# Optimization experiments

Measured on AMD Instinct MI355X. Metric: run time of the kernel, lower is better.

## Reference

```python
import math
import jax, jax.numpy as jnp
import numpy as np

N_HEAD = 16

def setup_inputs() -> dict:
    key = jax.random.key(0)
    k1, k2, k3 = jax.random.split(key, 3)
    B, T, C = 4, 2048, 1024
    x = jax.random.normal(k1, (B, T, C), dtype=jnp.float32)
    Wqkv = jax.random.normal(k2, (C, 3 * C), dtype=jnp.float32) * (1.0 / math.sqrt(C))
    bqkv = jnp.zeros((3 * C,), dtype=jnp.float32)
    Wproj = jax.random.normal(k3, (C, C), dtype=jnp.float32) * (1.0 / math.sqrt(C))
    bproj = jnp.zeros((C,), dtype=jnp.float32)
    return {"x": x, "Wqkv": Wqkv, "bqkv": bqkv, "Wproj": Wproj, "bproj": bproj}

def reference(x, Wqkv, bqkv, Wproj, bproj):
    B, T, C = x.shape
    H = N_HEAD
    D = C // H
    # fused QKV projection
    qkv = x @ Wqkv + bqkv                      # [B,T,3C]
    qkv = qkv.reshape(B, T, 3, H, D).transpose(0, 2, 3, 1, 4)  # [B,3,H,T,D]
    q, k, v = qkv[:, 0], qkv[:, 1], qkv[:, 2]  # each [B,H,T,D]
    scale = 1.0 / math.sqrt(D)
    att = jnp.einsum('bhtd,bhsd->bhts', q, k) * scale  # [B,H,T,T]
    # causal mask: disallow s > t
    mask = jnp.triu(jnp.ones((T, T), dtype=bool), k=1)
    att = jnp.where(mask, jnp.float32(-1e9), att)
    att = jax.nn.softmax(att, axis=-1)
    y = jnp.einsum('bhts,bhsd->bhtd', att, v)  # [B,H,T,D]
    y = y.transpose(0, 2, 1, 3).reshape(B, T, C)
    y = y @ Wproj + bproj
    return y
```

## Files before the change

kernel.cpp:

```cpp
#include <hip/hip_runtime.h>
#include <hip/hip_bf16.h>

#define B_ 4
#define T_ 2048
#define C_ 1024
#define H_ 16
#define D_ 64

typedef __attribute__((ext_vector_type(8))) short short8;
typedef __attribute__((ext_vector_type(4))) float f32x4;

#define QSCALE 0.18033688011112042f

static __device__ __forceinline__ unsigned short f2bf(float f) {
  unsigned u = __float_as_uint(f);
  u += 0x7fff + ((u >> 16) & 1);
  return (unsigned short)(u >> 16);
}

static __device__ __forceinline__ unsigned cvt_pk_bf16(float lo, float hi) {
  unsigned r;
  asm("v_cvt_pk_bf16_f32 %0, %1, %2" : "=v"(r) : "v"(lo), "v"(hi));
  return r;
}

static __device__ __forceinline__ float fast_exp2(float x) {
#if __has_builtin(__builtin_amdgcn_exp2f)
  return __builtin_amdgcn_exp2f(x);
#else
  return exp2f(x);
#endif
}

#define GL2LDS16(g, l)                                              \
  __builtin_amdgcn_global_load_lds(                                 \
      (const __attribute__((address_space(1))) void*)(g),           \
      (__attribute__((address_space(3))) void*)(l), 16, 0, 0)

__global__ __launch_bounds__(256) void prepass(
    const float* __restrict__ x, const float* __restrict__ Wq,
    const float* __restrict__ Wp, ushort* __restrict__ xb,
    ushort* __restrict__ Wqt, ushort* __restrict__ Wpt) {
  __shared__ ushort tile[32][33];
  const int bid = blockIdx.x;
  if (bid < 8192) {
    const size_t i = ((size_t)bid * 256 + threadIdx.x) * 4;
    float4 vv = *(const float4*)(x + i);
    ushort4 o = {f2bf(vv.x), f2bf(vv.y), f2bf(vv.z), f2bf(vv.w)};
    *(ushort4*)(xb + i) = o;
    return;
  }
  const float* in;
  ushort* out;
  int N, tix;
  if (bid < 8192 + 3072) {
    in = Wq; out = Wqt; N = 3 * C_; tix = bid - 8192;
  } else {
    in = Wp; out = Wpt; N = C_; tix = bid - 11264;
  }
  const int nT = N >> 5;
  const int k0 = (tix / nT) << 5, n0 = (tix % nT) << 5;
  const int r = threadIdx.x >> 3;
  const int c4 = (threadIdx.x & 7) << 2;
  float4 v = *(const float4*)(in + (size_t)(k0 + r) * N + n0 + c4);
  tile[c4 + 0][r] = f2bf(v.x);
  tile[c4 + 1][r] = f2bf(v.y);
  tile[c4 + 2][r] = f2bf(v.z);
  tile[c4 + 3][r] = f2bf(v.w);
  __syncthreads();
  ushort4 o = {tile[r][c4], tile[r][c4 + 1], tile[r][c4 + 2], tile[r][c4 + 3]};
  *(ushort4*)(out + (size_t)(n0 + r) * C_ + k0 + c4) = o;
}

static __device__ __forceinline__ void swz_src64(int wave, int lane, int p,
                                                 int& row, int& offU) {
  const int flat = p * 4096 + wave * 1024 + lane * 16;
  row = flat >> 7;
  const int pos = (flat & 127) >> 4;
  const int x = pos ^ (row & 7);
  offU = x * 8;
}
static __device__ __forceinline__ int swz_frag64(int r, int quad, int ko) {
  return r * 128 + (((quad | (ko << 2)) ^ (r & 7)) << 4);
}

__global__ __launch_bounds__(256) void gemm_qkv_mfma(
    const ushort* __restrict__ A, const ushort* __restrict__ Bt,
    const float* __restrict__ bias, ushort* __restrict__ q,
    ushort* __restrict__ k, ushort* __restrict__ v) {
  __shared__ __align__(16) ushort As[128 * 64];
  __shared__ __align__(16) ushort Bs[128 * 64];
  const int tid = threadIdx.x;
  const int wave = tid >> 6, lane = tid & 63;
  const int c = lane & 15, quad = lane >> 4;
  const int wm = wave & 1, wn = wave >> 1;
  const int bid0 = blockIdx.y * 24 + blockIdx.x;
  const int bid = (bid0 & 7) * 192 + (bid0 >> 3);
  const int m0 = (bid / 24) << 7;
  const int n0 = (bid % 24) << 7;

  int sRow[4], sOff[4];
#pragma unroll
  for (int p = 0; p < 4; ++p) swz_src64(wave, lane, p, sRow[p], sOff[p]);
  int fOffA[2][4], fOffB[2][4];
#pragma unroll
  for (int ko = 0; ko < 2; ++ko) {
#pragma unroll
    for (int i = 0; i < 4; ++i)
      fOffA[ko][i] = swz_frag64(wm * 64 + i * 16 + c, quad, ko);
#pragma unroll
    for (int j = 0; j < 4; ++j)
      fOffB[ko][j] = swz_frag64(wn * 64 + j * 16 + c, quad, ko);
  }

  f32x4 acc[4][4];
#pragma unroll
  for (int i = 0; i < 4; ++i)
#pragma unroll
    for (int j = 0; j < 4; ++j) acc[i][j] = (f32x4){0.f, 0.f, 0.f, 0.f};

  for (int k0 = 0; k0 < C_; k0 += 64) {
    __syncthreads();
#pragma unroll
    for (int p = 0; p < 4; ++p) {
      GL2LDS16(A + (size_t)(m0 + sRow[p]) * C_ + k0 + sOff[p],
               (char*)As + p * 4096 + wave * 1024);
      GL2LDS16(Bt + (size_t)(n0 + sRow[p]) * C_ + k0 + sOff[p],
               (char*)Bs + p * 4096 + wave * 1024);
    }
    __syncthreads();
#pragma unroll
    for (int ko = 0; ko < 2; ++ko) {
      short8 af[4], bf[4];
#pragma unroll
      for (int i = 0; i < 4; ++i)
        af[i] = *(const short8*)((const char*)As + fOffA[ko][i]);
#pragma unroll
      for (int j = 0; j < 4; ++j)
        bf[j] = *(const short8*)((const char*)Bs + fOffB[ko][j]);
#pragma unroll
      for (int i = 0; i < 4; ++i)
#pragma unroll
        for (int j = 0; j < 4; ++j)
          acc[i][j] = __builtin_amdgcn_mfma_f32_16x16x32_bf16(af[i], bf[j],
                                                              acc[i][j], 0, 0, 0);
    }
  }

  const int s = n0 >> 10;
  if (s == 2) {
#pragma unroll
    for (int j = 0; j < 4; ++j) {
      const int n = n0 + wn * 64 + j * 16 + c;
      const int h = (n >> 6) & 15, d = n & 63;
      const float bval = bias[n];
#pragma unroll
      for (int i = 0; i < 4; ++i) {
        const int m = m0 + wm * 64 + i * 16 + quad * 4;
        const int b = m >> 11, t = m & 2047;
        ushort4 pk = {f2bf(acc[i][j][0] + bval), f2bf(acc[i][j][1] + bval),
                      f2bf(acc[i][j][2] + bval), f2bf(acc[i][j][3] + bval)};
        *(ushort4*)(v + (((size_t)((b << 4) + h) << 6) + d) * T_ + t) = pk;
      }
    }
  } else {
    ushort* outp = (s == 0) ? q : k;
    const float sc = (s == 0) ? QSCALE : 1.0f;
#pragma unroll
    for (int j = 0; j < 4; ++j) {
      const int n = n0 + wn * 64 + j * 16 + c;
      const int h = (n >> 6) & 15, d = n & 63;
      const float bval = bias[n];
#pragma unroll
      for (int i = 0; i < 4; ++i) {
#pragma unroll
        for (int r = 0; r < 4; ++r) {
          const int m = m0 + wm * 64 + i * 16 + quad * 4 + r;
          const int b = m >> 11, t = m & 2047;
          outp[(((size_t)((b << 4) + h) << 11) + t) * 64 + d] =
              f2bf((acc[i][j][r] + bval) * sc);
        }
      }
    }
  }
}

__global__ __launch_bounds__(256) void gemm_proj_mfma(
    const ushort* __restrict__ A, const ushort* __restrict__ Bt,
    const float* __restrict__ bias, float* __restrict__ out) {
  __shared__ __align__(16) ushort As[128 * 64];
  __shared__ __align__(16) ushort Bs[128 * 64];
  const int tid = threadIdx.x;
  const int wave = tid >> 6, lane = tid & 63;
  const int c = lane & 15, quad = lane >> 4;
  const int wm = wave & 1, wn = wave >> 1;
  const int bid0 = blockIdx.y * 8 + blockIdx.x;
  const int bid = (bid0 & 7) * 64 + (bid0 >> 3);
  const int m0 = (bid >> 3) << 7;
  const int n0 = (bid & 7) << 7;

  int sRow[4], sOff[4];
#pragma unroll
  for (int p = 0; p < 4; ++p) swz_src64(wave, lane, p, sRow[p], sOff[p]);
  int fOffA[2][4], fOffB[2][4];
#pragma unroll
  for (int ko = 0; ko < 2; ++ko) {
#pragma unroll
    for (int i = 0; i < 4; ++i)
      fOffA[ko][i] = swz_frag64(wm * 64 + i * 16 + c, quad, ko);
#pragma unroll
    for (int j = 0; j < 4; ++j)
      fOffB[ko][j] = swz_frag64(wn * 64 + j * 16 + c, quad, ko);
  }

  f32x4 acc[4][4];
#pragma unroll
  for (int i = 0; i < 4; ++i)
#pragma unroll
    for (int j = 0; j < 4; ++j) acc[i][j] = (f32x4){0.f, 0.f, 0.f, 0.f};

  for (int k0 = 0; k0 < C_; k0 += 64) {
    __syncthreads();
#pragma unroll
    for (int p = 0; p < 4; ++p) {
      GL2LDS16(A + (size_t)(m0 + sRow[p]) * C_ + k0 + sOff[p],
               (char*)As + p * 4096 + wave * 1024);
      GL2LDS16(Bt + (size_t)(n0 + sRow[p]) * C_ + k0 + sOff[p],
               (char*)Bs + p * 4096 + wave * 1024);
    }
    __syncthreads();
#pragma unroll
    for (int ko = 0; ko < 2; ++ko) {
      short8 af[4], bf[4];
#pragma unroll
      for (int i = 0; i < 4; ++i)
        af[i] = *(const short8*)((const char*)As + fOffA[ko][i]);
#pragma unroll
      for (int j = 0; j < 4; ++j)
        bf[j] = *(const short8*)((const char*)Bs + fOffB[ko][j]);
#pragma unroll
      for (int i = 0; i < 4; ++i)
#pragma unroll
        for (int j = 0; j < 4; ++j)
          acc[i][j] = __builtin_amdgcn_mfma_f32_16x16x32_bf16(af[i], bf[j],
                                                              acc[i][j], 0, 0, 0);
    }
  }

#pragma unroll
  for (int j = 0; j < 4; ++j) {
    const int n = n0 + wn * 64 + j * 16 + c;
    const float bval = bias[n];
#pragma unroll
    for (int i = 0; i < 4; ++i) {
#pragma unroll
      for (int r = 0; r < 4; ++r) {
        const int m = m0 + wm * 64 + i * 16 + quad * 4 + r;
        out[(size_t)m * C_ + n] = acc[i][j][r] + bval;
      }
    }
  }
}

__global__ __launch_bounds__(256) void attn(const ushort* __restrict__ q,
                                            const ushort* __restrict__ k,
                                            const ushort* __restrict__ v,
                                            ushort* __restrict__ y2) {
  const int qt = 15 - (int)(blockIdx.x >> 6);
  const int bh = blockIdx.x & 63;
  const int t0 = qt << 7;
  const int w = threadIdx.x >> 6;
  const int lane = threadIdx.x & 63;
  const int c = lane & 15;
  const int quad = lane >> 4;

  const ushort* qp = q + (size_t)bh * T_ * D_;
  const ushort* kp = k + (size_t)bh * T_ * D_;
  const ushort* vp = v + (size_t)bh * D_ * T_;

  __shared__ __align__(16) ushort Ks[2][64 * 64];
  __shared__ __align__(16) ushort Vs[2][64 * 64];
  __shared__ __align__(16) ushort Ps[4][32][72];

  short8 qf[2][2];
#pragma unroll
  for (int g = 0; g < 2; ++g) {
    const ushort* qrow = qp + (size_t)(t0 + 32 * w + 16 * g + c) * D_;
    qf[g][0] = *(const short8*)(qrow + quad * 8);
    qf[g][1] = *(const short8*)(qrow + 32 + quad * 8);
  }

  int sRow[2], sX[2];
#pragma unroll
  for (int p = 0; p < 2; ++p) {
    const int flat = p * 4096 + (int)threadIdx.x * 16;
    sRow[p] = flat >> 7;
    sX[p] = (((flat & 127) >> 4) ^ (sRow[p] & 7)) * 8;
  }

#define STAGE(buf, s0s)                                                   \
  do {                                                                    \
    _Pragma("unroll") for (int p = 0; p < 2; ++p) {                       \
      GL2LDS16(kp + (size_t)((s0s) + sRow[p]) * D_ + sX[p],               \
               (char*)Ks[buf] + p * 4096 + w * 1024);                     \
      GL2LDS16(vp + (size_t)sRow[p] * T_ + (s0s) + sX[p],                 \
               (char*)Vs[buf] + p * 4096 + w * 1024);                     \
    }                                                                     \
  } while (0)

  f32x4 o[2][4];
  float l_i[2] = {0.f, 0.f};
#pragma unroll
  for (int g = 0; g < 2; ++g)
#pragma unroll
    for (int dt = 0; dt < 4; ++dt) o[g][dt] = (f32x4){0.f, 0.f, 0.f, 0.f};

  const int nb = 2 * qt + 2;
  STAGE(0, 0);
  int cur = 0;

  for (int ib = 0; ib < nb; ++ib) {
    const int s0 = ib << 6;
    __syncthreads();
    if (ib + 1 < nb) STAGE(cur ^ 1, s0 + 64);

    f32x4 st[2][4];
    __builtin_amdgcn_s_setprio(1);
#pragma unroll
    for (int kt = 0; kt < 4; ++kt) {
      const char* kb = (const char*)Ks[cur];
      short8 af0 = *(const short8*)(kb + swz_frag64(kt * 16 + c, quad, 0));
      short8 af1 = *(const short8*)(kb + swz_frag64(kt * 16 + c, quad, 1));
#pragma unroll
      for (int g = 0; g < 2; ++g) {
        f32x4 a = (f32x4){0.f, 0.f, 0.f, 0.f};
        a = __builtin_amdgcn_mfma_f32_16x16x32_bf16(af0, qf[g][0], a, 0, 0, 0);
        a = __builtin_amdgcn_mfma_f32_16x16x32_bf16(af1, qf[g][1], a, 0, 0, 0);
        st[g][kt] = a;
      }
    }
    __builtin_amdgcn_s_setprio(0);

#pragma unroll
    for (int g = 0; g < 2; ++g) {
      const int qbase = t0 + 32 * w + 16 * g;
      if (s0 + 63 > qbase) {
#pragma unroll
        for (int kt = 0; kt < 4; ++kt)
#pragma unroll
          for (int r = 0; r < 4; ++r)
            if (s0 + kt * 16 + 4 * quad + r > qbase + c) st[g][kt][r] = -1e30f;
      }
      float lacc = 0.f;
#pragma unroll
      for (int kt = 0; kt < 4; ++kt) {
        float p0 = fast_exp2(st[g][kt][0]);
        float p1 = fast_exp2(st[g][kt][1]);
        float p2 = fast_exp2(st[g][kt][2]);
        float p3 = fast_exp2(st[g][kt][3]);
        lacc += (p0 + p1) + (p2 + p3);
        uint2 pw = {cvt_pk_bf16(p0, p1), cvt_pk_bf16(p2, p3)};
        *(uint2*)(&Ps[w][g * 16 + c][kt * 16 + 4 * quad]) = pw;
      }
      l_i[g] += lacc;
    }

    short8 pf[2][2];
#pragma unroll
    for (int g = 0; g < 2; ++g) {
      pf[g][0] = *(const short8*)(&Ps[w][g * 16 + c][quad * 8]);
      pf[g][1] = *(const short8*)(&Ps[w][g * 16 + c][32 + quad * 8]);
    }
    __builtin_amdgcn_s_setprio(1);
#pragma unroll
    for (int dt = 0; dt < 4; ++dt) {
      const char* vb = (const char*)Vs[cur];
      short8 vf0 = *(const short8*)(vb + swz_frag64(dt * 16 + c, quad, 0));
      short8 vf1 = *(const short8*)(vb + swz_frag64(dt * 16 + c, quad, 1));
#pragma unroll
      for (int g = 0; g < 2; ++g) {
        o[g][dt] =
            __builtin_amdgcn_mfma_f32_16x16x32_bf16(vf0, pf[g][0], o[g][dt], 0, 0, 0);
        o[g][dt] =
            __builtin_amdgcn_mfma_f32_16x16x32_bf16(vf1, pf[g][1], o[g][dt], 0, 0, 0);
      }
    }
    __builtin_amdgcn_s_setprio(0);
    cur ^= 1;
  }
#undef STAGE

  float linv[2];
#pragma unroll
  for (int g = 0; g < 2; ++g) {
    float ls = l_i[g];
    ls += __shfl_xor(ls, 16);
    ls += __shfl_xor(ls, 32);
    linv[g] = 1.0f / ls;
  }

  const int b = bh >> 4, h = bh & 15;
#pragma unroll
  for (int g = 0; g < 2; ++g) {
    const int row = t0 + 32 * w + 16 * g + c;
    ushort* dst = y2 + (size_t)(b * T_ + row) * C_ + h * 64;
#pragma unroll
    for (int dt = 0; dt < 4; ++dt) {
      uint2 ov = {cvt_pk_bf16(o[g][dt][0] * linv[g], o[g][dt][1] * linv[g]),
                  cvt_pk_bf16(o[g][dt][2] * linv[g], o[g][dt][3] * linv[g])};
      *(uint2*)(dst + dt * 16 + 4 * quad) = ov;
    }
  }
}

extern "C" void kernel_launch(void* const* d_in, const int* in_sizes, int n_in,
                              void* d_out, int out_size, void* d_ws,
                              size_t ws_size, hipStream_t stream) {
  const float* x = (const float*)d_in[0];
  const float* Wqkv = (const float*)d_in[1];
  const float* bqkv = (const float*)d_in[2];
  const float* Wproj = (const float*)d_in[3];
  const float* bproj = (const float*)d_in[4];
  float* out = (float*)d_out;

  const size_t per = (size_t)B_ * H_ * T_ * D_;
  ushort* q = (ushort*)d_ws;
  ushort* k = q + per;
  ushort* v = k + per;
  ushort* y2 = v + per;
  ushort* xb = y2 + per;
  ushort* Wqkvt = xb + per;
  ushort* Wprojt = Wqkvt + 3 * C_ * C_;

  prepass<<<dim3(12288), 256, 0, stream>>>(x, Wqkv, Wproj, xb, Wqkvt, Wprojt);
  gemm_qkv_mfma<<<dim3(24, 64), 256, 0, stream>>>(xb, Wqkvt, bqkv, q, k, v);
  attn<<<dim3(1024), 256, 0, stream>>>(q, k, v, y2);
  gemm_proj_mfma<<<dim3(8, 64), 256, 0, stream>>>(y2, Wprojt, bproj, out);
}
```

Before: 244.2 us.

## Rewrite GEMM mainloops with triple-buffered LDS and 8-wave 128x256 tiles

Both projection GEMMs now use 512-thread blocks computing 128x256 output tiles, with a three-stage LDS ring buffer fed by global-to-LDS loads issued two k-steps ahead. The MFMA work is split into four quadrant phases, each bracketed by barriers and s_setprio, so the next tile's loads interleave with compute. The goal is to hide global memory latency and reuse each loaded A tile across twice as many columns. In exchange it uses much more LDS (144 KB per block), adds many barriers per iteration, and relies on hand-written vmcnt waits that must match the number of loads issued.

Result: slower. 256.1 us (+4.9%).

```diff
diff --git a/kernel.cpp b/kernel.cpp
--- a/kernel.cpp
+++ b/kernel.cpp
@@ -72,80 +72,153 @@
   *(ushort4*)(out + (size_t)(n0 + r) * C_ + k0 + c4) = o;
 }
 
-static __device__ __forceinline__ void swz_src64(int wave, int lane, int p,
-                                                 int& row, int& offU) {
-  const int flat = p * 4096 + wave * 1024 + lane * 16;
-  row = flat >> 7;
-  const int pos = (flat & 127) >> 4;
-  const int x = pos ^ (row & 7);
-  offU = x * 8;
-}
 static __device__ __forceinline__ int swz_frag64(int r, int quad, int ko) {
   return r * 128 + (((quad | (ko << 2)) ^ (r & 7)) << 4);
 }
 
-__global__ __launch_bounds__(256) void gemm_qkv_mfma(
+#define GEMM_MAINLOOP(A_, B_ptr, KA_, KB_)                                     \
+  int aRow[2], aX[2], bRow[4], bX[4];                                          \
+  _Pragma("unroll") for (int p = 0; p < 2; ++p) {                              \
+    const int flat = p * 8192 + (int)threadIdx.x * 16;                         \
+    aRow[p] = flat >> 7;                                                       \
+    aX[p] = (((flat & 127) >> 4) ^ (aRow[p] & 7)) * 8;                         \
+  }                                                                            \
+  _Pragma("unroll") for (int p = 0; p < 4; ++p) {                              \
+    const int flat = p * 8192 + (int)threadIdx.x * 16;                         \
+    bRow[p] = flat >> 7;                                                       \
+    bX[p] = (((flat & 127) >> 4) ^ (bRow[p] & 7)) * 8;                         \
+  }                                                                            \
+  int fOffA[2][4], fOffB[2][4];                                                \
+  _Pragma("unroll") for (int ko = 0; ko < 2; ++ko) {                           \
+    _Pragma("unroll") for (int i = 0; i < 4; ++i)                              \
+        fOffA[ko][i] = swz_frag64(wm * 64 + i * 16 + c, quad, ko);             \
+    _Pragma("unroll") for (int j = 0; j < 4; ++j)                              \
+        fOffB[ko][j] = swz_frag64(wn * 64 + j * 16 + c, quad, ko);             \
+  }                                                                            \
+  _Pragma("unroll") for (int i = 0; i < 4; ++i)                                \
+      _Pragma("unroll") for (int j = 0; j < 4; ++j) acc[i][j] =                \
+          (f32x4){0.f, 0.f, 0.f, 0.f};                                         \
+              \
+  _Pragma("unroll") for (int p = 0; p < 4; ++p)                                \
+      GL2LDS16(B_ptr + (size_t)(n0 + bRow[p]) * C_ + bX[p],                    \
+               (char*)KB_[0] + p * 8192 + wave * 1024);                        \
+  _Pragma("unroll") for (int p = 0; p < 2; ++p)                                \
+      GL2LDS16(A_ + (size_t)(m0 + aRow[p]) * C_ + aX[p],                       \
+               (char*)KA_[0] + p * 8192 + wave * 1024);                        \
+  _Pragma("unroll") for (int p = 0; p < 4; ++p)                                \
+      GL2LDS16(B_ptr + (size_t)(n0 + bRow[p]) * C_ + 64 + bX[p],               \
+               (char*)KB_[1] + p * 8192 + wave * 1024);                        \
+  _Pragma("unroll") for (int p = 0; p < 2; ++p)                                \
+      GL2LDS16(A_ + (size_t)(m0 + aRow[p]) * C_ + 64 + aX[p],                  \
+               (char*)KA_[1] + p * 8192 + wave * 1024);                        \
+  asm volatile("s_waitcnt vmcnt(6)" ::: "memory");                             \
+  __builtin_amdgcn_s_barrier();                                                \
+  int cur = 0, s2 = 2;                                                         \
+  for (int kt = 0; kt < 16; ++kt) {                                            \
+    const int kk2 = (kt + 2) << 6;                                             \
+    const bool more = (kt + 2) < 16;                                           \
+    const char* la = (const char*)KA_[cur];                                    \
+    const char* lb = (const char*)KB_[cur];                                    \
+    short8 af0[2][2], af1[2][2], bf0[2][2], bf1[2][2];                         \
+         \
+    _Pragma("unroll") for (int d = 0; d < 2; ++d)                              \
+        _Pragma("unroll") for (int ko = 0; ko < 2; ++ko) {                     \
+      af0[d][ko] = *(const short8*)(la + fOffA[ko][d]);                        \
+      bf0[d][ko] = *(const short8*)(lb + fOffB[ko][d]);                        \
+    }                                                                          \
+    if (more) {                                                                \
+      GL2LDS16(B_ptr + (size_t)(n0 + bRow[0]) * C_ + kk2 + bX[0],              \
+               (char*)KB_[s2] + 0 * 8192 + wave * 1024);                       \
+      GL2LDS16(B_ptr + (size_t)(n0 + bRow[1]) * C_ + kk2 + bX[1],              \
+               (char*)KB_[s2] + 1 * 8192 + wave * 1024);                       \
+    }                                                                          \
+    __builtin_amdgcn_s_barrier();                                              \
+    __builtin_amdgcn_s_setprio(1);                                             \
+    _Pragma("unroll") for (int di = 0; di < 2; ++di)                           \
+        _Pragma("unroll") for (int dj = 0; dj < 2; ++dj)                       \
+            _Pragma("unroll") for (int ko = 0; ko < 2; ++ko) acc[di][dj] =     \
+                __builtin_amdgcn_mfma_f32_16x16x32_bf16(                       \
+                    af0[di][ko], bf0[dj][ko], acc[di][dj], 0, 0, 0);           \
+    __builtin_amdgcn_s_setprio(0);                                             \
+    __builtin_amdgcn_s_barrier();                                              \
+               \
+    _Pragma("unroll") for (int d = 0; d < 2; ++d)                              \
+        _Pragma("unroll") for (int ko = 0; ko < 2; ++ko) bf1[d][ko] =          \
+            *(const short8*)(lb + fOffB[ko][2 + d]);                           \
+    if (more) {                                                                \
+      GL2LDS16(B_ptr + (size_t)(n0 + bRow[2]) * C_ + kk2 + bX[2],              \
+               (char*)KB_[s2] + 2 * 8192 + wave * 1024);                       \
+      GL2LDS16(B_ptr + (size_t)(n0 + bRow[3]) * C_ + kk2 + bX[3],              \
+               (char*)KB_[s2] + 3 * 8192 + wave * 1024);                       \
+    }                                                                          \
+    __builtin_amdgcn_s_barrier();                                              \
+    __builtin_amdgcn_s_setprio(1);                                             \
+    _Pragma("unroll") for (int di = 0; di < 2; ++di)                           \
+        _Pragma("unroll") for (int dj = 0; dj < 2; ++dj)                       \
+            _Pragma("unroll") for (int ko = 0; ko < 2; ++ko) acc[di][2 + dj] = \
+                __builtin_amdgcn_mfma_f32_16x16x32_bf16(                       \
+                    af0[di][ko], bf1[dj][ko], acc[di][2 + dj], 0, 0, 0);       \
+    __builtin_amdgcn_s_setprio(0);                                             \
+    __builtin_amdgcn_s_barrier();                                              \
+                  \
+    _Pragma("unroll") for (int d = 0; d < 2; ++d)                              \
+        _Pragma("unroll") for (int ko = 0; ko < 2; ++ko) af1[d][ko] =          \
+            *(const short8*)(la + fOffA[ko][2 + d]);                           \
+    if (more)                                                                  \
+      GL2LDS16(A_ + (size_t)(m0 + aRow[0]) * C_ + kk2 + aX[0],                 \
+               (char*)KA_[s2] + 0 * 8192 + wave * 1024);                       \
+    __builtin_amdgcn_s_barrier();                                              \
+    __builtin_amdgcn_s_setprio(1);                                             \
+    _Pragma("unroll") for (int di = 0; di < 2; ++di)                           \
+        _Pragma("unroll") for (int dj = 0; dj < 2; ++dj)                       \
+            _Pragma("unroll") for (int ko = 0; ko < 2; ++ko)                   \
+                acc[2 + di][2 + dj] =                                          \
+                    __builtin_amdgcn_mfma_f32_16x16x32_bf16(                   \
+                        af1[di][ko], bf1[dj][ko], acc[2 + di][2 + dj], 0, 0,   \
+                        0);                                                    \
+    __builtin_amdgcn_s_setprio(0);                                             \
+    __builtin_amdgcn_s_barrier();                                              \
+                  \
+    if (more)                                                                  \
+      GL2LDS16(A_ + (size_t)(m0 + aRow[1]) * C_ + kk2 + aX[1],                 \
+               (char*)KA_[s2] + 1 * 8192 + wave * 1024);                       \
+    __builtin_amdgcn_s_barrier();                                              \
+    __builtin_amdgcn_s_setprio(1);                                             \
+    _Pragma("unroll") for (int di = 0; di < 2; ++di)                           \
+        _Pragma("unroll") for (int dj = 0; dj < 2; ++dj)                       \
+            _Pragma("unroll") for (int ko = 0; ko < 2; ++ko) acc[2 + di][dj] = \
+                __builtin_amdgcn_mfma_f32_16x16x32_bf16(                       \
+                    af1[di][ko], bf0[dj][ko], acc[2 + di][dj], 0, 0, 0);       \
+    __builtin_amdgcn_s_setprio(0);                                             \
+    __builtin_amdgcn_s_barrier();                                              \
+                               \
+    if (kt + 1 < 16) {                                                         \
+      if (more)                                                                \
+        asm volatile("s_waitcnt vmcnt(6)" ::: "memory");                       \
+      else                                                                     \
+        asm volatile("s_waitcnt vmcnt(0)" ::: "memory");                       \
+      __builtin_amdgcn_s_barrier();                                            \
+    }                                                                          \
+    cur = (cur == 2) ? 0 : cur + 1;                                            \
+    s2 = (s2 == 2) ? 0 : s2 + 1;                                               \
+  }
+
+__global__ __launch_bounds__(512, 2) void gemm_qkv_mfma(
     const ushort* __restrict__ A, const ushort* __restrict__ Bt,
     const float* __restrict__ bias, ushort* __restrict__ q,
     ushort* __restrict__ k, ushort* __restrict__ v) {
-  __shared__ __align__(16) ushort As[128 * 64];
-  __shared__ __align__(16) ushort Bs[128 * 64];
-  const int tid = threadIdx.x;
-  const int wave = tid >> 6, lane = tid & 63;
+  __shared__ __align__(16) ushort KA[3][128 * 64];
+  __shared__ __align__(16) ushort KB[3][256 * 64];
+  const int wave = threadIdx.x >> 6, lane = threadIdx.x & 63;
   const int c = lane & 15, quad = lane >> 4;
-  const int wm = wave & 1, wn = wave >> 1;
-  const int bid0 = blockIdx.y * 24 + blockIdx.x;
-  const int bid = (bid0 & 7) * 192 + (bid0 >> 3);
-  const int m0 = (bid / 24) << 7;
-  const int n0 = (bid % 24) << 7;
-
-  int sRow[4], sOff[4];
-#pragma unroll
-  for (int p = 0; p < 4; ++p) swz_src64(wave, lane, p, sRow[p], sOff[p]);
-  int fOffA[2][4], fOffB[2][4];
-#pragma unroll
-  for (int ko = 0; ko < 2; ++ko) {
-#pragma unroll
-    for (int i = 0; i < 4; ++i)
-      fOffA[ko][i] = swz_frag64(wm * 64 + i * 16 + c, quad, ko);
-#pragma unroll
-    for (int j = 0; j < 4; ++j)
-      fOffB[ko][j] = swz_frag64(wn * 64 + j * 16 + c, quad, ko);
-  }
+  const int wm = wave >> 2, wn = wave & 3;
+  const int bid0 = blockIdx.x;
+  const int bid = (bid0 & 7) * 96 + (bid0 >> 3);
+  const int m0 = (bid / 12) << 7;
+  const int n0 = (bid % 12) << 8;
 
   f32x4 acc[4][4];
-#pragma unroll
-  for (int i = 0; i < 4; ++i)
-#pragma unroll
-    for (int j = 0; j < 4; ++j) acc[i][j] = (f32x4){0.f, 0.f, 0.f, 0.f};
-
-  for (int k0 = 0; k0 < C_; k0 += 64) {
-    __syncthreads();
-#pragma unroll
-    for (int p = 0; p < 4; ++p) {
-      GL2LDS16(A + (size_t)(m0 + sRow[p]) * C_ + k0 + sOff[p],
-               (char*)As + p * 4096 + wave * 1024);
-      GL2LDS16(Bt + (size_t)(n0 + sRow[p]) * C_ + k0 + sOff[p],
-               (char*)Bs + p * 4096 + wave * 1024);
-    }
-    __syncthreads();
-#pragma unroll
-    for (int ko = 0; ko < 2; ++ko) {
-      short8 af[4], bf[4];
-#pragma unroll
-      for (int i = 0; i < 4; ++i)
-        af[i] = *(const short8*)((const char*)As + fOffA[ko][i]);
-#pragma unroll
-      for (int j = 0; j < 4; ++j)
-        bf[j] = *(const short8*)((const char*)Bs + fOffB[ko][j]);
-#pragma unroll
-      for (int i = 0; i < 4; ++i)
-#pragma unroll
-        for (int j = 0; j < 4; ++j)
-          acc[i][j] = __builtin_amdgcn_mfma_f32_16x16x32_bf16(af[i], bf[j],
-                                                              acc[i][j], 0, 0, 0);
-    }
-  }
+  GEMM_MAINLOOP(A, Bt, KA, KB)
 
   const int s = n0 >> 10;
   if (s == 2) {
@@ -185,67 +258,21 @@
   }
 }
 
-__global__ __launch_bounds__(256) void gemm_proj_mfma(
+__global__ __launch_bounds__(512, 2) void gemm_proj_mfma(
     const ushort* __restrict__ A, const ushort* __restrict__ Bt,
     const float* __restrict__ bias, float* __restrict__ out) {
-  __shared__ __align__(16) ushort As[128 * 64];
-  __shared__ __align__(16) ushort Bs[128 * 64];
-  const int tid = threadIdx.x;
-  const int wave = tid >> 6, lane = tid & 63;
+  __shared__ __align__(16) ushort KA[3][128 * 64];
+  __shared__ __align__(16) ushort KB[3][256 * 64];
+  const int wave = threadIdx.x >> 6, lane = threadIdx.x & 63;
   const int c = lane & 15, quad = lane >> 4;
-  const int wm = wave & 1, wn = wave >> 1;
-  const int bid0 = blockIdx.y * 8 + blockIdx.x;
-  const int bid = (bid0 & 7) * 64 + (bid0 >> 3);
-  const int m0 = (bid >> 3) << 7;
-  const int n0 = (bid & 7) << 7;
-
-  int sRow[4], sOff[4];
-#pragma unroll
-  for (int p = 0; p < 4; ++p) swz_src64(wave, lane, p, sRow[p], sOff[p]);
-  int fOffA[2][4], fOffB[2][4];
-#pragma unroll
-  for (int ko = 0; ko < 2; ++ko) {
-#pragma unroll
-    for (int i = 0; i < 4; ++i)
-      fOffA[ko][i] = swz_frag64(wm * 64 + i * 16 + c, quad, ko);
-#pragma unroll
-    for (int j = 0; j < 4; ++j)
-      fOffB[ko][j] = swz_frag64(wn * 64 + j * 16 + c, quad, ko);
-  }
+  const int wm = wave >> 2, wn = wave & 3;
+  const int bid0 = blockIdx.x;
+  const int bid = (bid0 & 7) * 32 + (bid0 >> 3);
+  const int m0 = (bid >> 2) << 7;
+  const int n0 = (bid & 3) << 8;
 
   f32x4 acc[4][4];
-#pragma unroll
-  for (int i = 0; i < 4; ++i)
-#pragma unroll
-    for (int j = 0; j < 4; ++j) acc[i][j] = (f32x4){0.f, 0.f, 0.f, 0.f};
-
-  for (int k0 = 0; k0 < C_; k0 += 64) {
-    __syncthreads();
-#pragma unroll
-    for (int p = 0; p < 4; ++p) {
-      GL2LDS16(A + (size_t)(m0 + sRow[p]) * C_ + k0 + sOff[p],
-               (char*)As + p * 4096 + wave * 1024);
-      GL2LDS16(Bt + (size_t)(n0 + sRow[p]) * C_ + k0 + sOff[p],
-               (char*)Bs + p * 4096 + wave * 1024);
-    }
-    __syncthreads();
-#pragma unroll
-    for (int ko = 0; ko < 2; ++ko) {
-      short8 af[4], bf[4];
-#pragma unroll
-      for (int i = 0; i < 4; ++i)
-        af[i] = *(const short8*)((const char*)As + fOffA[ko][i]);
-#pragma unroll
-      for (int j = 0; j < 4; ++j)
-        bf[j] = *(const short8*)((const char*)Bs + fOffB[ko][j]);
-#pragma unroll
-      for (int i = 0; i < 4; ++i)
-#pragma unroll
-        for (int j = 0; j < 4; ++j)
-          acc[i][j] = __builtin_amdgcn_mfma_f32_16x16x32_bf16(af[i], bf[j],
-                                                              acc[i][j], 0, 0, 0);
-    }
-  }
+  GEMM_MAINLOOP(A, Bt, KA, KB)
 
 #pragma unroll
   for (int j = 0; j < 4; ++j) {
@@ -433,7 +460,7 @@
   ushort* Wprojt = Wqkvt + 3 * C_ * C_;
 
   prepass<<<dim3(12288), 256, 0, stream>>>(x, Wqkv, Wproj, xb, Wqkvt, Wprojt);
-  gemm_qkv_mfma<<<dim3(24, 64), 256, 0, stream>>>(xb, Wqkvt, bqkv, q, k, v);
+  gemm_qkv_mfma<<<dim3(768), 512, 0, stream>>>(xb, Wqkvt, bqkv, q, k, v);
   attn<<<dim3(1024), 256, 0, stream>>>(q, k, v, y2);
-  gemm_proj_mfma<<<dim3(8, 64), 256, 0, stream>>>(y2, Wprojt, bproj, out);
-}
+  gemm_proj_mfma<<<dim3(256), 512, 0, stream>>>(y2, Wprojt, bproj, out);
+}
```

## Pipeline QKV GEMM with triple-buffered LDS and 128x256 tiles over 8 waves

Applied to the files above, without the earlier changes.

Rewrites the QKV projection GEMM to use 512-thread blocks computing 128x256 output tiles, with a three-stage LDS ring buffer. Global-to-LDS loads for step k+2 are issued in two halves, each interleaved with a half of the MFMA work, using explicit vmcnt waits, raw barriers and setprio. This targets the load/compute serialization of the previous two-barrier, single-buffer loop. It needs more LDS per block (144 KB), which limits occupancy and relies on hand-tuned waitcnt counts being correct.

Measured after the change: 258.8 us. +6.0%, slower.

```diff
diff --git a/kernel.cpp b/kernel.cpp
--- a/kernel.cpp
+++ b/kernel.cpp
@@ -84,24 +84,33 @@
   return r * 128 + (((quad | (ko << 2)) ^ (r & 7)) << 4);
 }
 
-__global__ __launch_bounds__(256) void gemm_qkv_mfma(
+__global__ __launch_bounds__(512, 2) void gemm_qkv_mfma(
     const ushort* __restrict__ A, const ushort* __restrict__ Bt,
     const float* __restrict__ bias, ushort* __restrict__ q,
     ushort* __restrict__ k, ushort* __restrict__ v) {
-  __shared__ __align__(16) ushort As[128 * 64];
-  __shared__ __align__(16) ushort Bs[128 * 64];
-  const int tid = threadIdx.x;
-  const int wave = tid >> 6, lane = tid & 63;
+  __shared__ __align__(16) ushort KA[3][128 * 64];
+  __shared__ __align__(16) ushort KB[3][256 * 64];
+  const int wave = threadIdx.x >> 6, lane = threadIdx.x & 63;
   const int c = lane & 15, quad = lane >> 4;
-  const int wm = wave & 1, wn = wave >> 1;
-  const int bid0 = blockIdx.y * 24 + blockIdx.x;
-  const int bid = (bid0 & 7) * 192 + (bid0 >> 3);
-  const int m0 = (bid / 24) << 7;
-  const int n0 = (bid % 24) << 7;
-
-  int sRow[4], sOff[4];
-#pragma unroll
-  for (int p = 0; p < 4; ++p) swz_src64(wave, lane, p, sRow[p], sOff[p]);
+  const int wm = wave >> 2, wn = wave & 3;
+  const int bid0 = blockIdx.x;
+  const int bid = (bid0 & 7) * 96 + (bid0 >> 3);
+  const int m0 = (bid / 12) << 7;
+  const int n0 = (bid % 12) << 8;
+
+  int aRow[2], aX[2], bRow[4], bX[4];
+#pragma unroll
+  for (int p = 0; p < 2; ++p) {
+    const int flat = p * 8192 + (int)threadIdx.x * 16;
+    aRow[p] = flat >> 7;
+    aX[p] = (((flat & 127) >> 4) ^ (aRow[p] & 7)) * 8;
+  }
+#pragma unroll
+  for (int p = 0; p < 4; ++p) {
+    const int flat = p * 8192 + (int)threadIdx.x * 16;
+    bRow[p] = flat >> 7;
+    bX[p] = (((flat & 127) >> 4) ^ (bRow[p] & 7)) * 8;
+  }
   int fOffA[2][4], fOffB[2][4];
 #pragma unroll
   for (int ko = 0; ko < 2; ++ko) {
@@ -119,32 +128,97 @@
 #pragma unroll
     for (int j = 0; j < 4; ++j) acc[i][j] = (f32x4){0.f, 0.f, 0.f, 0.f};
 
-  for (int k0 = 0; k0 < C_; k0 += 64) {
-    __syncthreads();
-#pragma unroll
-    for (int p = 0; p < 4; ++p) {
-      GL2LDS16(A + (size_t)(m0 + sRow[p]) * C_ + k0 + sOff[p],
-               (char*)As + p * 4096 + wave * 1024);
-      GL2LDS16(Bt + (size_t)(n0 + sRow[p]) * C_ + k0 + sOff[p],
-               (char*)Bs + p * 4096 + wave * 1024);
-    }
-    __syncthreads();
-#pragma unroll
-    for (int ko = 0; ko < 2; ++ko) {
-      short8 af[4], bf[4];
-#pragma unroll
-      for (int i = 0; i < 4; ++i)
-        af[i] = *(const short8*)((const char*)As + fOffA[ko][i]);
-#pragma unroll
-      for (int j = 0; j < 4; ++j)
-        bf[j] = *(const short8*)((const char*)Bs + fOffB[ko][j]);
-#pragma unroll
-      for (int i = 0; i < 4; ++i)
-#pragma unroll
-        for (int j = 0; j < 4; ++j)
-          acc[i][j] = __builtin_amdgcn_mfma_f32_16x16x32_bf16(af[i], bf[j],
-                                                              acc[i][j], 0, 0, 0);
-    }
+#pragma unroll
+  for (int p = 0; p < 4; ++p)
+    GL2LDS16(Bt + (size_t)(n0 + bRow[p]) * C_ + bX[p],
+             (char*)KB[0] + p * 8192 + wave * 1024);
+#pragma unroll
+  for (int p = 0; p < 2; ++p)
+    GL2LDS16(A + (size_t)(m0 + aRow[p]) * C_ + aX[p],
+             (char*)KA[0] + p * 8192 + wave * 1024);
+#pragma unroll
+  for (int p = 0; p < 4; ++p)
+    GL2LDS16(Bt + (size_t)(n0 + bRow[p]) * C_ + 64 + bX[p],
+             (char*)KB[1] + p * 8192 + wave * 1024);
+#pragma unroll
+  for (int p = 0; p < 2; ++p)
+    GL2LDS16(A + (size_t)(m0 + aRow[p]) * C_ + 64 + aX[p],
+             (char*)KA[1] + p * 8192 + wave * 1024);
+  asm volatile("s_waitcnt vmcnt(6)" ::: "memory");
+  __builtin_amdgcn_s_barrier();
+
+  int cur = 0, s2 = 2;
+  for (int kt = 0; kt < 16; ++kt) {
+    const int kk2 = (kt + 2) << 6;
+    const bool more = (kt + 2) < 16;
+    const char* la = (const char*)KA[cur];
+    const char* lb = (const char*)KB[cur];
+    short8 af[4][2], bf0[2][2], bf1[2][2];
+
+#pragma unroll
+    for (int i = 0; i < 4; ++i)
+#pragma unroll
+      for (int ko = 0; ko < 2; ++ko) af[i][ko] = *(const short8*)(la + fOffA[ko][i]);
+#pragma unroll
+    for (int d = 0; d < 2; ++d)
+#pragma unroll
+      for (int ko = 0; ko < 2; ++ko) bf0[d][ko] = *(const short8*)(lb + fOffB[ko][d]);
+    if (more) {
+      GL2LDS16(Bt + (size_t)(n0 + bRow[0]) * C_ + kk2 + bX[0],
+               (char*)KB[s2] + 0 * 8192 + wave * 1024);
+      GL2LDS16(Bt + (size_t)(n0 + bRow[1]) * C_ + kk2 + bX[1],
+               (char*)KB[s2] + 1 * 8192 + wave * 1024);
+      GL2LDS16(A + (size_t)(m0 + aRow[0]) * C_ + kk2 + aX[0],
+               (char*)KA[s2] + 0 * 8192 + wave * 1024);
+    }
+    __builtin_amdgcn_s_barrier();
+    __builtin_amdgcn_s_setprio(1);
+#pragma unroll
+    for (int i = 0; i < 4; ++i)
+#pragma unroll
+      for (int dj = 0; dj < 2; ++dj)
+#pragma unroll
+        for (int ko = 0; ko < 2; ++ko)
+          acc[i][dj] = __builtin_amdgcn_mfma_f32_16x16x32_bf16(
+              af[i][ko], bf0[dj][ko], acc[i][dj], 0, 0, 0);
+    __builtin_amdgcn_s_setprio(0);
+    __builtin_amdgcn_s_barrier();
+
+#pragma unroll
+    for (int d = 0; d < 2; ++d)
+#pragma unroll
+      for (int ko = 0; ko < 2; ++ko)
+        bf1[d][ko] = *(const short8*)(lb + fOffB[ko][2 + d]);
+    if (more) {
+      GL2LDS16(Bt + (size_t)(n0 + bRow[2]) * C_ + kk2 + bX[2],
+               (char*)KB[s2] + 2 * 8192 + wave * 1024);
+      GL2LDS16(Bt + (size_t)(n0 + bRow[3]) * C_ + kk2 + bX[3],
+               (char*)KB[s2] + 3 * 8192 + wave * 1024);
+      GL2LDS16(A + (size_t)(m0 + aRow[1]) * C_ + kk2 + aX[1],
+               (char*)KA[s2] + 1 * 8192 + wave * 1024);
+    }
+    __builtin_amdgcn_s_barrier();
+    __builtin_amdgcn_s_setprio(1);
+#pragma unroll
+    for (int i = 0; i < 4; ++i)
+#pragma unroll
+      for (int dj = 0; dj < 2; ++dj)
+#pragma unroll
+        for (int ko = 0; ko < 2; ++ko)
+          acc[i][2 + dj] = __builtin_amdgcn_mfma_f32_16x16x32_bf16(
+              af[i][ko], bf1[dj][ko], acc[i][2 + dj], 0, 0, 0);
+    __builtin_amdgcn_s_setprio(0);
+    __builtin_amdgcn_s_barrier();
+
+    if (kt + 1 < 16) {
+      if (more)
+        asm volatile("s_waitcnt vmcnt(6)" ::: "memory");
+      else
+        asm volatile("s_waitcnt vmcnt(0)" ::: "memory");
+      __builtin_amdgcn_s_barrier();
+    }
+    cur = (cur == 2) ? 0 : cur + 1;
+    s2 = (s2 == 2) ? 0 : s2 + 1;
   }
 
   const int s = n0 >> 10;
@@ -433,7 +507,7 @@
   ushort* Wprojt = Wqkvt + 3 * C_ * C_;
 
   prepass<<<dim3(12288), 256, 0, stream>>>(x, Wqkv, Wproj, xb, Wqkvt, Wprojt);
-  gemm_qkv_mfma<<<dim3(24, 64), 256, 0, stream>>>(xb, Wqkvt, bqkv, q, k, v);
+  gemm_qkv_mfma<<<dim3(768), 512, 0, stream>>>(xb, Wqkvt, bqkv, q, k, v);
   attn<<<dim3(1024), 256, 0, stream>>>(q, k, v, y2);
   gemm_proj_mfma<<<dim3(8, 64), 256, 0, stream>>>(y2, Wprojt, bproj, out);
 }
```
